# Optimization experiments

Hardware: AMD Instinct MI355X
Metric: run time of the kernel (lower is better)

## Reference

```python
import jax, jax.numpy as jnp
import numpy as np

BS, S, E, H = 64, 512, 1024, 16
HD = E // H
MASK_ID, KNOW_ID = 30001, 30002


def setup_inputs() -> dict:
    key = jax.random.key(0)
    ks = jax.random.split(key, 8)
    model_output = jax.random.normal(ks[0], (BS, S, E), dtype=jnp.float32)
    ids = jax.random.randint(ks[1], (BS, S), 0, 30000)  # never hits special ids
    ids = ids.at[:, 0].set(MASK_ID)        # exactly one [MASK] per sequence
    ids = ids.at[:, 1:9].set(KNOW_ID)      # 8 knowledge slots per sequence
    knowledge_output = jax.random.normal(ks[2], (BS, E), dtype=jnp.float32)
    empty_knowledge_mask = jax.random.randint(ks[3], (BS,), 0, 2).astype(bool)
    bound = 1.0 / np.sqrt(E)
    in_proj_weight = jax.random.uniform(ks[4], (3 * E, E), minval=-bound, maxval=bound, dtype=jnp.float32)
    in_proj_bias = jnp.zeros((3 * E,), jnp.float32)
    out_proj_weight = jax.random.uniform(ks[5], (E, E), minval=-bound, maxval=bound, dtype=jnp.float32)
    out_proj_bias = jnp.zeros((E,), jnp.float32)
    attention_strength = jnp.float32(0.1)
    return {
        "model_output": model_output,
        "knowledge_output": knowledge_output,
        "in_proj_weight": in_proj_weight,
        "in_proj_bias": in_proj_bias,
        "out_proj_weight": out_proj_weight,
        "out_proj_bias": out_proj_bias,
        "attention_strength": attention_strength,
        "input_ids": ids,
        "empty_knowledge_mask": empty_knowledge_mask,
        "knowledge_token_id": KNOW_ID,
        "mask_token_id": MASK_ID,
    }


def reference(model_output, knowledge_output, in_proj_weight, in_proj_bias,
              out_proj_weight, out_proj_bias, attention_strength,
              input_ids, empty_knowledge_mask, knowledge_token_id, mask_token_id):
    bs, sent_len, hidden = model_output.shape
    # --- knowledge injection: scatter knowledge vector into knowledge-token slots ---
    knowledge_mask = input_ids == knowledge_token_id                 # [bs, S]
    kv_src = jnp.where(knowledge_mask[:, :, None],
                       knowledge_output[:, None, :], model_output)  # [bs, S, E]
    # --- single-query gather: one [MASK] position per sequence ---
    mask_pos = jnp.argmax(input_ids == mask_token_id, axis=1)        # [bs]
    q_in = jnp.take_along_axis(kv_src, mask_pos[:, None, None], axis=1)[:, 0, :]  # [bs, E]
    # --- nn.MultiheadAttention (eval mode, dropout=0) ---
    Wq, Wk, Wv = in_proj_weight[:E], in_proj_weight[E:2 * E], in_proj_weight[2 * E:]
    bq, bk, bv = in_proj_bias[:E], in_proj_bias[E:2 * E], in_proj_bias[2 * E:]
    q = (q_in @ Wq.T + bq).reshape(bs, H, HD)                        # [bs, H, hd]
    k = (kv_src @ Wk.T + bk).reshape(bs, sent_len, H, HD)            # [bs, S, H, hd]
    v = (kv_src @ Wv.T + bv).reshape(bs, sent_len, H, HD)
    scale = 1.0 / np.sqrt(HD)
    scores = jnp.einsum('bhd,bshd->bhs', q * scale, k)               # [bs, H, S]
    attn = jax.nn.softmax(scores, axis=-1)
    ctx = jnp.einsum('bhs,bshd->bhd', attn, v).reshape(bs, hidden)   # [bs, E]
    attn_output = ctx @ out_proj_weight.T + out_proj_bias            # [bs, E]
    # --- residual on the ORIGINAL (pre-injection) mask-token states ---
    origin_q = jnp.take_along_axis(model_output, mask_pos[:, None, None], axis=1)[:, 0, :]
    mask_output = origin_q + attention_strength * attn_output
    # --- conditional restore where knowledge is empty ---
    mask_output = jnp.where(empty_knowledge_mask[:, None], origin_q, mask_output)
    return mask_output
```

## Files before the change

### kernel.cpp

```cpp
#include <hip/hip_runtime.h>

#define BS 64
#define S  512
#define E  1024
#define H  16
#define HD 64
#define SCALE 0.125f
#define CATT 8

#define W_QKBF 66560
#define W_NUM  1115136
#define W_DEN  9503744
#define W_CTX  9511936

typedef __attribute__((ext_vector_type(8))) short short8;
typedef __attribute__((ext_vector_type(4))) float floatx4;

union S8u { uint2 u2[2]; short8 s; };

__device__ __forceinline__ unsigned short bf16c(float x) {
    unsigned int u = __float_as_uint(x);
    return (unsigned short)((u + 0x7fffu + ((u >> 16) & 1u)) >> 16);
}
__device__ __forceinline__ unsigned int pack_bf16(float a, float b) {
    return (unsigned int)bf16c(a) | ((unsigned int)bf16c(b) << 16);
}
__device__ __forceinline__ void fma4(float4& acc, float s, const float4& v) {
    acc.x += s * v.x; acc.y += s * v.y; acc.z += s * v.z; acc.w += s * v.w;
}
__device__ __forceinline__ float dot4(const float4& a, const float4& b) {
    return a.x * b.x + a.y * b.y + a.z * b.z + a.w * b.w;
}
__device__ __forceinline__ void bfly8(float* a) {
    #pragma unroll
    for (int off = 32; off > 0; off >>= 1) {
        #pragma unroll
        for (int i = 0; i < 8; i++) a[i] += __shfl_xor(a[i], off, 64);
    }
}

__global__ void k_qgen(const float* __restrict__ model, const float* __restrict__ knowledge,
                       const int* __restrict__ ids, const int* __restrict__ mask_id_p,
                       const int* __restrict__ kid_p, int* __restrict__ mp,
                       const float* __restrict__ w_in, const float* __restrict__ b_in,
                       unsigned short* __restrict__ qkbf) {
    int h = blockIdx.x, b0 = blockIdx.y * 4, t = threadIdx.x;
    __shared__ float qin_l[4][1024];
    __shared__ float qred[4][64][4];
    __shared__ float qs_l[4][64];
    __shared__ int best[4];
    if (t < 4) best[t] = S;
    __syncthreads();
    {
        int bb = t >> 6, ls = t & 63;
        int mid = mask_id_p[0];
        int found = S;
        #pragma unroll
        for (int k = 0; k < 8; k++) {
            int s = ls + k * 64;
            if (ids[(size_t)(b0 + bb) * S + s] == mid) found = min(found, s);
        }
        if (found < S) atomicMin(&best[bb], found);
    }
    __syncthreads();
    {
        int kid = kid_p[0];
        #pragma unroll
        for (int bb = 0; bb < 4; bb++) {
            int m = (best[bb] == S) ? 0 : best[bb];
            bool isk = (ids[(size_t)(b0 + bb) * S + m] == kid);
            const float* qrow = isk ? knowledge + (size_t)(b0 + bb) * E
                                    : model + ((size_t)((b0 + bb) * S + m)) * E;
            *(float4*)&qin_l[bb][t * 4] = *(const float4*)(qrow + t * 4);
        }
        if (h == 0 && t < 4) mp[b0 + t] = (best[t] == S) ? 0 : best[t];
    }
    __syncthreads();
    {
        int d = t >> 2, part = t & 3;
        const float* wr = w_in + (size_t)(h * HD + d) * E + part * 256;
        float acc[4] = {0.f, 0.f, 0.f, 0.f};
        #pragma unroll 8
        for (int i = 0; i < 64; i++) {
            float4 wv = *(const float4*)(wr + i * 4);
            #pragma unroll
            for (int bb = 0; bb < 4; bb++)
                acc[bb] += dot4(wv, *(const float4*)&qin_l[bb][part * 256 + i * 4]);
        }
        #pragma unroll
        for (int bb = 0; bb < 4; bb++) qred[bb][d][part] = acc[bb];
    }
    __syncthreads();
    if (t < 64) {
        float bias = b_in[h * HD + t];
        #pragma unroll
        for (int bb = 0; bb < 4; bb++)
            qs_l[bb][t] = qred[bb][t][0] + qred[bb][t][1] + qred[bb][t][2] + qred[bb][t][3] + bias;
    }
    __syncthreads();
    {
        int e0 = t * 4;
        const float* wk = w_in + (size_t)(E + h * HD) * E + e0;
        float4 acc[4];
        #pragma unroll
        for (int bb = 0; bb < 4; bb++) acc[bb] = make_float4(0.f, 0.f, 0.f, 0.f);
        #pragma unroll 8
        for (int d = 0; d < HD; d++) {
            float4 wv = *(const float4*)(wk + (size_t)d * E);
            #pragma unroll
            for (int bb = 0; bb < 4; bb++) fma4(acc[bb], qs_l[bb][d], wv);
        }
        #pragma unroll
        for (int bb = 0; bb < 4; bb++) {
            uint2 pk;
            pk.x = pack_bf16(acc[bb].x * SCALE, acc[bb].y * SCALE);
            pk.y = pack_bf16(acc[bb].z * SCALE, acc[bb].w * SCALE);
            *(uint2*)&qkbf[((size_t)(b0 + bb) * H + h) * E + e0] = pk;
        }
    }
}

__global__ __launch_bounds__(512, 4) void k_attn(
    const float* __restrict__ model, const float* __restrict__ knowledge,
    const int* __restrict__ ids, const int* __restrict__ kid_p,
    const int* __restrict__ empty,
    const unsigned short* __restrict__ qkbf, unsigned short* __restrict__ num,
    float* __restrict__ den) {
    int c = blockIdx.x, b = blockIdx.y;
    if (empty[b]) return;

    __shared__ __align__(16) unsigned char Ubuf[73984];
    unsigned short* Rbuf  = (unsigned short*)Ubuf;
    unsigned short* RbufT = (unsigned short*)(Ubuf + 33024);
    unsigned short* TbufH = (unsigned short*)Ubuf;
    __shared__ unsigned short Pbuf[16 * 40];
    __shared__ float Sred[4][16][17];
    __shared__ float denp[4][16];
    __shared__ unsigned long long kmask_s;

    int tid = threadIdx.x;
    int w = tid >> 6, l = tid & 63;
    int quad = l >> 4, lm = l & 15;
    int s0 = c * 64;

    if (w == 0) {
        int id = ids[b * S + s0 + l];
        unsigned long long mk = __ballot(id == kid_p[0]);
        if (l == 0) kmask_s = mk;
    }
    floatx4 accn[8];
    #pragma unroll
    for (int i = 0; i < 8; i++) accn[i] = (floatx4)0.f;
    float accden = 0.f;
    const float* kb = knowledge + (size_t)b * E;
    const float* mb = model + (size_t)b * S * E;
    const unsigned short* qh = qkbf + ((size_t)b * H + lm) * E;
    __syncthreads();
    unsigned long long kmask = kmask_s;

    int rgA = tid >> 8;
    int c4  = tid & 255;

    float4 st[8];

    auto ISSUE = [&](int pass) {
        int rb = pass * 16;
        #pragma unroll
        for (int j = 0; j < 4; j++) {
            int row = rb + rgA * 4 + j;
            const float* rp = ((kmask >> row) & 1ull) ? kb : mb + (size_t)(s0 + row) * E;
            st[j] = *(const float4*)(rp + c4 * 4);
        }
        #pragma unroll
        for (int j = 0; j < 4; j++) {
            int row = rb + (rgA + 2) * 4 + j;
            const float* rp = ((kmask >> row) & 1ull) ? kb : mb + (size_t)(s0 + row) * E;
            st[4 + j] = *(const float4*)(rp + c4 * 4);
        }
    };
    auto STORE = [&]() {
        #pragma unroll
        for (int u = 0; u < 2; u++) {
            int rg = rgA + u * 2;
            unsigned short hh[4][4];
            #pragma unroll
            for (int j = 0; j < 4; j++) {
                float4 v = st[u * 4 + j];
                hh[j][0] = bf16c(v.x); hh[j][1] = bf16c(v.y);
                hh[j][2] = bf16c(v.z); hh[j][3] = bf16c(v.w);
            }
            #pragma unroll
            for (int j = 0; j < 4; j++) {
                uint2 pk;
                pk.x = (unsigned int)hh[j][0] | ((unsigned int)hh[j][1] << 16);
                pk.y = (unsigned int)hh[j][2] | ((unsigned int)hh[j][3] << 16);
                *(uint2*)&Rbuf[(rg * 4 + j) * 1032 + c4 * 4] = pk;
            }
            #pragma unroll
            for (int k = 0; k < 4; k++) {
                uint2 pk;
                pk.x = (unsigned int)hh[0][k] | ((unsigned int)hh[1][k] << 16);
                pk.y = (unsigned int)hh[2][k] | ((unsigned int)hh[3][k] << 16);
                *(uint2*)&RbufT[(c4 * 4 + k) * 20 + rg * 4] = pk;
            }
        }
    };

    ISSUE(0);
    STORE();
    __syncthreads();

    #pragma unroll
    for (int pass = 0; pass < 4; pass++) {
        if (pass < 3) ISSUE(pass + 1);
        if (w < 4) {
            floatx4 acs = (floatx4)0.f;
            #pragma unroll
            for (int t = 0; t < 8; t++) {
                int kk = w * 8 + t;
                short8 a  = *(const short8*)(const void*)&Rbuf[lm * 1032 + kk * 32 + quad * 8];
                short8 bf = *(const short8*)(const void*)(qh + kk * 32 + quad * 8);
                acs = __builtin_amdgcn_mfma_f32_16x16x32_bf16(a, bf, acs, 0, 0, 0);
            }
            Sred[w][quad * 4 + 0][lm] = acs[0];
            Sred[w][quad * 4 + 1][lm] = acs[1];
            Sred[w][quad * 4 + 2][lm] = acs[2];
            Sred[w][quad * 4 + 3][lm] = acs[3];
        }
        __syncthreads();
        if (w < 4) {
            int row = w * 4 + quad;
            float s = Sred[0][row][lm] + Sred[1][row][lm] + Sred[2][row][lm] + Sred[3][row][lm];
            float ex = __expf(s);
            accden += ex;
            Pbuf[lm * 40 + row] = bf16c(ex);
        }
        __syncthreads();
        {
            short8 afr = {};
            if (quad < 2) afr = *(const short8*)(const void*)&Pbuf[lm * 40 + quad * 8];
            #pragma unroll
            for (int i = 0; i < 8; i++) {
                int e = (w * 8 + i) * 16 + lm;
                S8u bb2; bb2.s = (short8){};
                if (quad < 2) {
                    bb2.u2[0] = *(const uint2*)&RbufT[e * 20 + quad * 8];
                    bb2.u2[1] = *(const uint2*)&RbufT[e * 20 + quad * 8 + 4];
                }
                accn[i] = __builtin_amdgcn_mfma_f32_16x16x32_bf16(afr, bb2.s, accn[i], 0, 0, 0);
            }
        }
        __syncthreads();
        if (pass < 3) {
            STORE();
            __syncthreads();
        }
    }
    #pragma unroll
    for (int i = 0; i < 8; i++) {
        int e = (w * 8 + i) * 16 + lm;
        TbufH[(quad * 4 + 0) * 1024 + e] = bf16c(accn[i][0]);
        TbufH[(quad * 4 + 1) * 1024 + e] = bf16c(accn[i][1]);
        TbufH[(quad * 4 + 2) * 1024 + e] = bf16c(accn[i][2]);
        TbufH[(quad * 4 + 3) * 1024 + e] = bf16c(accn[i][3]);
    }
    if (w < 4) {
        accden += __shfl_xor(accden, 16, 64);
        accden += __shfl_xor(accden, 32, 64);
        if (l < 16) denp[w][l] = accden;
    }
    __syncthreads();
    if (w == 0 && l < 16)
        den[(size_t)(c * BS + b) * H + l] = denp[0][l] + denp[1][l] + denp[2][l] + denp[3][l];
    uint4* numv = (uint4*)(num + ((size_t)(c * BS + b) * H) * E);
    const uint4* tb = (const uint4*)TbufH;
    #pragma unroll
    for (int k = 0; k < 4; k++)
        numv[k * 512 + tid] = tb[k * 512 + tid];
}

__global__ void k_pc(const unsigned short* __restrict__ num, const float* __restrict__ den,
                     const int* __restrict__ empty,
                     const float* __restrict__ w_in, const float* __restrict__ b_in,
                     float* __restrict__ ctx) {
    int h = blockIdx.x, b0 = blockIdx.y * 4, t = threadIdx.x;
    __shared__ float p_l[4][1024];
    __shared__ float cred[4][64][4];
    __shared__ float inv_l[4];
    #pragma unroll
    for (int k = 0; k < 2; k++) {
        int idx8 = k * 256 + t;
        int bb = idx8 >> 7, e8 = (idx8 & 127) * 8;
        float a0 = 0.f, a1 = 0.f, a2 = 0.f, a3 = 0.f, a4 = 0.f, a5 = 0.f, a6 = 0.f, a7 = 0.f;
        if (!empty[b0 + bb]) {
            #pragma unroll
            for (int cc = 0; cc < CATT; cc++) {
                uint4 v = *(const uint4*)(num + (((size_t)(cc * BS + b0 + bb) * H + h) * E) + e8);
                a0 += __uint_as_float(v.x << 16);
                a1 += __uint_as_float(v.x & 0xffff0000u);
                a2 += __uint_as_float(v.y << 16);
                a3 += __uint_as_float(v.y & 0xffff0000u);
                a4 += __uint_as_float(v.z << 16);
                a5 += __uint_as_float(v.z & 0xffff0000u);
                a6 += __uint_as_float(v.w << 16);
                a7 += __uint_as_float(v.w & 0xffff0000u);
            }
        }
        *(float4*)&p_l[bb][e8]     = make_float4(a0, a1, a2, a3);
        *(float4*)&p_l[bb][e8 + 4] = make_float4(a4, a5, a6, a7);
    }
    if (t < 4) {
        float iv = 0.f;
        if (!empty[b0 + t]) {
            float ds = 0.f;
            for (int cc = 0; cc < CATT; cc++) ds += den[(size_t)(cc * BS + b0 + t) * H + h];
            iv = 1.0f / ds;
        }
        inv_l[t] = iv;
    }
    __syncthreads();
    {
        int jj = t >> 2, part = t & 3;
        const float* wr = w_in + (size_t)(2 * E + h * HD + jj) * E + part * 256;
        float acc[4] = {0.f, 0.f, 0.f, 0.f};
        #pragma unroll 8
        for (int i = 0; i < 64; i++) {
            float4 wv = *(const float4*)(wr + i * 4);
            #pragma unroll
            for (int bb = 0; bb < 4; bb++)
                acc[bb] += dot4(wv, *(const float4*)&p_l[bb][part * 256 + i * 4]);
        }
        #pragma unroll
        for (int bb = 0; bb < 4; bb++) cred[bb][jj][part] = acc[bb];
    }
    __syncthreads();
    if (t < 64) {
        float bias = b_in[2 * E + h * HD + t];
        #pragma unroll
        for (int bb = 0; bb < 4; bb++) {
            float s = cred[bb][t][0] + cred[bb][t][1] + cred[bb][t][2] + cred[bb][t][3];
            ctx[(size_t)(b0 + bb) * E + h * HD + t] = inv_l[bb] * s + bias;
        }
    }
}

__global__ void k_out(const float* __restrict__ model, const float* __restrict__ w_out,
                      const float* __restrict__ b_out, const float* __restrict__ ctx,
                      const int* __restrict__ mp, const int* __restrict__ empty,
                      const float* __restrict__ strength_p, float* __restrict__ out) {
    int w = threadIdx.x >> 6, l = threadIdx.x & 63;
    int j = blockIdx.x * 4 + w;
    int b0 = blockIdx.y * 8;
    const float* wr = w_out + (size_t)j * E;
    float4 wv[4];
    #pragma unroll
    for (int r = 0; r < 4; r++) wv[r] = *(const float4*)(wr + r * 256 + l * 4);
    float acc[8];
    #pragma unroll
    for (int bb = 0; bb < 8; bb++) {
        const float* src = ctx + (size_t)(b0 + bb) * E;
        float a = 0.f;
        #pragma unroll
        for (int r = 0; r < 4; r++) a += dot4(wv[r], *(const float4*)(src + r * 256 + l * 4));
        acc[bb] = a;
    }
    bfly8(acc);
    if (l < 8) {
        float myacc = acc[0];
        #pragma unroll
        for (int bb = 1; bb < 8; bb++) myacc = (l == bb) ? acc[bb] : myacc;
        int b = b0 + l;
        int m = mp[b];
        float orig = model[((size_t)(b * S + m)) * E + j];
        float bias = b_out[j];
        float st = strength_p[0];
        out[(size_t)b * E + j] = empty[b] ? orig : orig + st * (myacc + bias);
    }
}

extern "C" void kernel_launch(void* const* d_in, const int* in_sizes, int n_in,
                              void* d_out, int out_size, void* d_ws, size_t ws_size,
                              hipStream_t stream) {
    const float* model     = (const float*)d_in[0];
    const float* knowledge = (const float*)d_in[1];
    const float* w_in      = (const float*)d_in[2];
    const float* b_in      = (const float*)d_in[3];
    const float* w_out     = (const float*)d_in[4];
    const float* b_out     = (const float*)d_in[5];
    const float* strength  = (const float*)d_in[6];
    const int*   ids       = (const int*)d_in[7];
    const int*   empty     = (const int*)d_in[8];
    const int*   know_id   = (const int*)d_in[9];
    const int*   mask_id   = (const int*)d_in[10];
    float* out = (float*)d_out;

    float* ws  = (float*)d_ws;
    int*   mp  = (int*)d_ws;
    unsigned short* qkbf = (unsigned short*)(ws + W_QKBF);
    unsigned short* num  = (unsigned short*)(ws + W_NUM);
    float* den = ws + W_DEN;
    float* ctx = ws + W_CTX;

    k_qgen<<<dim3(H, 16), 256, 0, stream>>>(model, knowledge, ids, mask_id, know_id, mp,
                                            w_in, b_in, qkbf);
    k_attn<<<dim3(CATT, BS), 512, 0, stream>>>(model, knowledge, ids, know_id, empty,
                                               qkbf, num, den);
    k_pc<<<dim3(H, 16), 256, 0, stream>>>(num, den, empty, w_in, b_in, ctx);
    k_out<<<dim3(256, 8), 256, 0, stream>>>(model, w_out, b_out, ctx, mp, empty, strength, out);
}
```

Measured before the change: 267.9 us.

## Reduce split-sequence partial sums with fp32 atomics instead of per-chunk bf16 buffers

Instead of each attention chunk block writing its own bf16 numerator slice and denominator to workspace for k_pc to sum over 8 chunks, blocks now atomically add fp32 partials into one per-batch buffer, zeroed in k_qgen. This removes the 8x partial-buffer write and read traffic and the bf16 rounding of partials. In exchange it issues many global float atomics (16K per block) with contention across the 8 chunk blocks per batch, and the summation order becomes nondeterministic.

New measurement: 276.8 us. 3.3% more time.

```diff
diff --git a/kernel.cpp b/kernel.cpp
--- a/kernel.cpp
+++ b/kernel.cpp
@@ -10,8 +10,8 @@
 
 #define W_QKBF 66560
 #define W_NUM  1115136
-#define W_DEN  9503744
-#define W_CTX  9511936
+#define W_DEN  2163712
+#define W_CTX  2164736
 
 typedef __attribute__((ext_vector_type(8))) short short8;
 typedef __attribute__((ext_vector_type(4))) float floatx4;
@@ -43,12 +43,20 @@
                        const int* __restrict__ ids, const int* __restrict__ mask_id_p,
                        const int* __restrict__ kid_p, int* __restrict__ mp,
                        const float* __restrict__ w_in, const float* __restrict__ b_in,
-                       unsigned short* __restrict__ qkbf) {
+                       unsigned short* __restrict__ qkbf,
+                       float* __restrict__ num, float* __restrict__ den) {
     int h = blockIdx.x, b0 = blockIdx.y * 4, t = threadIdx.x;
     __shared__ float qin_l[4][1024];
     __shared__ float qred[4][64][4];
     __shared__ float qs_l[4][64];
     __shared__ int best[4];
+    {
+        float4 z = make_float4(0.f, 0.f, 0.f, 0.f);
+        float4* nz = (float4*)num + (size_t)(blockIdx.y * H + h) * 1024;
+        #pragma unroll
+        for (int k = 0; k < 4; k++) nz[k * 256 + t] = z;
+        if (h == 0 && t < 64) den[blockIdx.y * 64 + t] = 0.f;
+    }
     if (t < 4) best[t] = S;
     __syncthreads();
     {
@@ -124,7 +132,7 @@
     const float* __restrict__ model, const float* __restrict__ knowledge,
     const int* __restrict__ ids, const int* __restrict__ kid_p,
     const int* __restrict__ empty,
-    const unsigned short* __restrict__ qkbf, unsigned short* __restrict__ num,
+    const unsigned short* __restrict__ qkbf, float* __restrict__ num,
     float* __restrict__ den) {
     int c = blockIdx.x, b = blockIdx.y;
     if (empty[b]) return;
@@ -132,7 +140,6 @@
     __shared__ __align__(16) unsigned char Ubuf[73984];
     unsigned short* Rbuf  = (unsigned short*)Ubuf;
     unsigned short* RbufT = (unsigned short*)(Ubuf + 33024);
-    unsigned short* TbufH = (unsigned short*)Ubuf;
     __shared__ unsigned short Pbuf[16 * 40];
     __shared__ float Sred[4][16][17];
     __shared__ float denp[4][16];
@@ -256,13 +263,15 @@
             __syncthreads();
         }
     }
-    #pragma unroll
-    for (int i = 0; i < 8; i++) {
-        int e = (w * 8 + i) * 16 + lm;
-        TbufH[(quad * 4 + 0) * 1024 + e] = bf16c(accn[i][0]);
-        TbufH[(quad * 4 + 1) * 1024 + e] = bf16c(accn[i][1]);
-        TbufH[(quad * 4 + 2) * 1024 + e] = bf16c(accn[i][2]);
-        TbufH[(quad * 4 + 3) * 1024 + e] = bf16c(accn[i][3]);
+    {
+        float* nb = num + (size_t)b * H * E;
+        #pragma unroll
+        for (int i = 0; i < 8; i++) {
+            int e = (w * 8 + i) * 16 + lm;
+            #pragma unroll
+            for (int j = 0; j < 4; j++)
+                atomicAdd(&nb[(size_t)(quad * 4 + j) * E + e], accn[i][j]);
+        }
     }
     if (w < 4) {
         accden += __shfl_xor(accden, 16, 64);
@@ -271,15 +280,10 @@
     }
     __syncthreads();
     if (w == 0 && l < 16)
-        den[(size_t)(c * BS + b) * H + l] = denp[0][l] + denp[1][l] + denp[2][l] + denp[3][l];
-    uint4* numv = (uint4*)(num + ((size_t)(c * BS + b) * H) * E);
-    const uint4* tb = (const uint4*)TbufH;
-    #pragma unroll
-    for (int k = 0; k < 4; k++)
-        numv[k * 512 + tid] = tb[k * 512 + tid];
-}
-
-__global__ void k_pc(const unsigned short* __restrict__ num, const float* __restrict__ den,
+        atomicAdd(&den[(size_t)b * H + l], denp[0][l] + denp[1][l] + denp[2][l] + denp[3][l]);
+}
+
+__global__ void k_pc(const float* __restrict__ num, const float* __restrict__ den,
                      const int* __restrict__ empty,
                      const float* __restrict__ w_in, const float* __restrict__ b_in,
                      float* __restrict__ ctx) {
@@ -291,31 +295,18 @@
     for (int k = 0; k < 2; k++) {
         int idx8 = k * 256 + t;
         int bb = idx8 >> 7, e8 = (idx8 & 127) * 8;
-        float a0 = 0.f, a1 = 0.f, a2 = 0.f, a3 = 0.f, a4 = 0.f, a5 = 0.f, a6 = 0.f, a7 = 0.f;
+        float4 a0 = make_float4(0.f, 0.f, 0.f, 0.f), a1 = a0;
         if (!empty[b0 + bb]) {
-            #pragma unroll
-            for (int cc = 0; cc < CATT; cc++) {
-                uint4 v = *(const uint4*)(num + (((size_t)(cc * BS + b0 + bb) * H + h) * E) + e8);
-                a0 += __uint_as_float(v.x << 16);
-                a1 += __uint_as_float(v.x & 0xffff0000u);
-                a2 += __uint_as_float(v.y << 16);
-                a3 += __uint_as_float(v.y & 0xffff0000u);
-                a4 += __uint_as_float(v.z << 16);
-                a5 += __uint_as_float(v.z & 0xffff0000u);
-                a6 += __uint_as_float(v.w << 16);
-                a7 += __uint_as_float(v.w & 0xffff0000u);
-            }
-        }
-        *(float4*)&p_l[bb][e8]     = make_float4(a0, a1, a2, a3);
-        *(float4*)&p_l[bb][e8 + 4] = make_float4(a4, a5, a6, a7);
+            const float* src = num + ((size_t)(b0 + bb) * H + h) * E + e8;
+            a0 = *(const float4*)src;
+            a1 = *(const float4*)(src + 4);
+        }
+        *(float4*)&p_l[bb][e8]     = a0;
+        *(float4*)&p_l[bb][e8 + 4] = a1;
     }
     if (t < 4) {
         float iv = 0.f;
-        if (!empty[b0 + t]) {
-            float ds = 0.f;
-            for (int cc = 0; cc < CATT; cc++) ds += den[(size_t)(cc * BS + b0 + t) * H + h];
-            iv = 1.0f / ds;
-        }
+        if (!empty[b0 + t]) iv = 1.0f / den[(size_t)(b0 + t) * H + h];
         inv_l[t] = iv;
     }
     __syncthreads();
@@ -397,12 +388,12 @@
     float* ws  = (float*)d_ws;
     int*   mp  = (int*)d_ws;
     unsigned short* qkbf = (unsigned short*)(ws + W_QKBF);
-    unsigned short* num  = (unsigned short*)(ws + W_NUM);
+    float* num = ws + W_NUM;
     float* den = ws + W_DEN;
     float* ctx = ws + W_CTX;
 
     k_qgen<<<dim3(H, 16), 256, 0, stream>>>(model, knowledge, ids, mask_id, know_id, mp,
-                                            w_in, b_in, qkbf);
+                                            w_in, b_in, qkbf, num, den);
     k_attn<<<dim3(CATT, BS), 512, 0, stream>>>(model, knowledge, ids, know_id, empty,
                                                qkbf, num, den);
     k_pc<<<dim3(H, 16), 256, 0, stream>>>(num, den, empty, w_in, b_in, ctx);
```
